# Kernel optimization log

Hardware: AMD Instinct MI355X
Metric: run time of the kernel (lower is better)

Reference implementation:

```python
import jax, jax.numpy as jnp
from jax import lax
import numpy as np

LATENT = 512
LABEL = 128
BATCH = 1024


def _maxpool2(x):
    # 2x2 max pool, stride 2, NCHW
    return lax.reduce_window(x, -jnp.inf, lax.max, (1, 1, 2, 2), (1, 1, 2, 2), 'VALID')


def _encoder(x, c1w, c1b, c2w, c2b, fw, fb):
    dn = ('NCHW', 'OIHW', 'NCHW')
    y = lax.conv_general_dilated(x, c1w, (1, 1), 'SAME', dimension_numbers=dn)
    y = _maxpool2(jax.nn.relu(y + c1b[None, :, None, None]))  # [B,32,14,14]
    y = lax.conv_general_dilated(y, c2w, (1, 1), 'SAME', dimension_numbers=dn)
    y = _maxpool2(jax.nn.relu(y + c2b[None, :, None, None]))  # [B,64,7,7]
    y = y.reshape(y.shape[0], -1)                              # [B,3136]
    return y @ fw.T + fb                                       # [B,latent]


def _hopfield_w(rep):
    # rho = mean over ALL elements (matches torch.mean(x))
    rho = jnp.mean(rep)
    t = rep - rho                      # [label, latent]
    w = t.T @ t                        # sum of rank-1 outer products
    w = w * (1.0 - jnp.eye(w.shape[0], dtype=w.dtype))  # zero diagonal
    return w / LABEL


def _clustering(lat, w):
    # batched fixed-length Hopfield relaxation with min-energy tracking
    s0 = jnp.tanh(lat)                 # [B,L]
    B = s0.shape[0]

    def step(carry, _):
        s, min_e, min_s = carry
        prev = lax.stop_gradient(s)    # torch detaches prev_s each iter
        s_new = jnp.abs(prev) * jnp.sign(prev @ w.T)      # [B,L]
        e = -jnp.einsum('bi,ij,bj->b', s_new, w, s_new)    # [B]
        better = e < min_e
        min_e = jnp.where(better, e, min_e)
        min_s = jnp.where(better[:, None], s_new, min_s)
        return (s_new, min_e, min_s), None

    init = (s0, jnp.full((B,), jnp.inf, dtype=s0.dtype), jnp.zeros_like(s0))
    (_, _, min_s), _ = lax.scan(step, init, None, length=LATENT)
    return min_s


def setup_inputs() -> dict:
    key = jax.random.key(0)
    ks = jax.random.split(key, 11)
    d = {}
    d['image'] = jax.random.normal(ks[0], (BATCH, 1, 28, 28), dtype=jnp.float32)
    d['label_images'] = jax.random.uniform(ks[1], (LABEL, 1, 28, 28), dtype=jnp.float32)
    d['conv1_w'] = jax.random.normal(ks[2], (32, 1, 5, 5), dtype=jnp.float32) * 0.1
    d['conv1_b'] = jnp.zeros((32,), dtype=jnp.float32)
    d['conv2_w'] = jax.random.normal(ks[3], (64, 32, 5, 5), dtype=jnp.float32) * 0.05
    d['conv2_b'] = jnp.zeros((64,), dtype=jnp.float32)
    d['fc1_w'] = jax.random.normal(ks[4], (LATENT, 64 * 7 * 7), dtype=jnp.float32) * 0.02
    d['fc1_b'] = jnp.zeros((LATENT,), dtype=jnp.float32)
    d['fcn_w'] = jax.random.normal(ks[5], (LABEL, LATENT), dtype=jnp.float32) * 0.05
    d['fcn_b'] = jnp.zeros((LABEL,), dtype=jnp.float32)
    return d


def reference(image, label_images, conv1_w, conv1_b, conv2_w, conv2_b,
              fc1_w, fc1_b, fcn_w, fcn_b):
    rep = jnp.tanh(_encoder(label_images, conv1_w, conv1_b, conv2_w, conv2_b, fc1_w, fc1_b))  # [label,L]
    lat = _encoder(image, conv1_w, conv1_b, conv2_w, conv2_b, fc1_w, fc1_b)                    # [B,L]
    # FCN on detached latents (torch: .clone().detach())
    label = jax.nn.softmax(lax.stop_gradient(lat) @ fcn_w.T + fcn_b, axis=1)                   # [B,label]
    w = _hopfield_w(rep)                                                                        # [L,L]
    min_s = _clustering(lat, w)                                                                 # [B,L]
    out = jax.nn.softmax(jnp.abs(min_s @ rep.T), axis=1)                                        # [B,label]
    return (out, label)
```

## Files before the change

### kernel.cpp

```cpp
#include <hip/hip_runtime.h>
#include <hip/hip_bf16.h>
#include <math.h>

#define BATCH 1024
#define LABEL 128
#define LATENT 512
#define NTOT 1152

typedef short short8 __attribute__((ext_vector_type(8)));
typedef float f32x16 __attribute__((ext_vector_type(16)));

__device__ __forceinline__ unsigned short f2bf(float f) {
    __hip_bfloat16 h = __float2bfloat16(f);
    return *(unsigned short*)&h;
}
__device__ __forceinline__ float bf2f(unsigned short u) {
    __hip_bfloat16 h; *(unsigned short*)&h = u;
    return __bfloat162float(h);
}

#define BSTR ((size_t)512 * 3136)
#define ASTR ((size_t)NTOT * 3136)
#define A2STR ((size_t)BATCH * 512)
#define W2STR ((size_t)LABEL * 512)


__global__ __launch_bounds__(256) void conv1_pool(const float* __restrict__ image,
                                                  const float* __restrict__ limg,
                                                  const float* __restrict__ wt,
                                                  const float* __restrict__ bias,
                                                  unsigned short* __restrict__ o1b) {
    const int n = blockIdx.x;
    const float* in = (n < BATCH) ? (image + (size_t)n * 784)
                                  : (limg + (size_t)(n - BATCH) * 784);
    __shared__ float pin[32][32];
    __shared__ float wts[32 * 25];
    const int tid = threadIdx.x;
    unsigned short* ob = o1b + (size_t)n * 12800;
    for (int i = tid; i < 256; i += 256) {
        int pl_ = i >> 7, r = i & 127;
        ob[pl_ * 6400 + 6272 + r] = 0;
    }
    for (int idx = tid; idx < 32 * 32; idx += 256) ((float*)pin)[idx] = 0.f;
    __syncthreads();
    for (int idx = tid; idx < 784; idx += 256) {
        int y = idx / 28, x = idx % 28;
        pin[y + 2][x + 2] = in[idx];
    }
    for (int idx = tid; idx < 800; idx += 256) wts[idx] = wt[idx];
    __syncthreads();
    const int oc = tid & 31;
    float wk[25];
    #pragma unroll
    for (int k = 0; k < 25; ++k) wk[k] = wts[oc * 25 + k];
    const float b = bias[oc];
    const int slot_lo = (oc & 7);
    const int gq = oc >> 3;
    for (int it = 0; it < 2; ++it) {
        const int py = (tid >> 5) + it * 8;
        if (py >= 14) continue;
        #pragma unroll
        for (int xh = 0; xh < 2; ++xh) {
            const int acol = xh ? 12 : 0;
            const int off = xh ? 2 : 0;
            float a0[14], a1[14];
            #pragma unroll
            for (int c = 0; c < 14; ++c) { a0[c] = b; a1[c] = b; }
            #pragma unroll
            for (int t = 0; t < 6; ++t) {
                float row[20];
                const float4* rp = (const float4*)&pin[2 * py + t][acol];
                #pragma unroll
                for (int v = 0; v < 5; ++v) {
                    float4 f = rp[v];
                    row[4 * v] = f.x; row[4 * v + 1] = f.y;
                    row[4 * v + 2] = f.z; row[4 * v + 3] = f.w;
                }
                if (t < 5) {
                    #pragma unroll
                    for (int kx = 0; kx < 5; ++kx) {
                        float w0 = wk[t * 5 + kx];
                        #pragma unroll
                        for (int c = 0; c < 14; ++c)
                            a0[c] = fmaf(row[c + kx + off], w0, a0[c]);
                    }
                }
                if (t >= 1) {
                    #pragma unroll
                    for (int kx = 0; kx < 5; ++kx) {
                        float w1 = wk[(t - 1) * 5 + kx];
                        #pragma unroll
                        for (int c = 0; c < 14; ++c)
                            a1[c] = fmaf(row[c + kx + off], w1, a1[c]);
                    }
                }
            }
            #pragma unroll
            for (int px = 0; px < 7; ++px) {
                float v = fmaxf(fmaxf(a0[2 * px], a0[2 * px + 1]),
                                fmaxf(a1[2 * px], a1[2 * px + 1]));
                v = fmaxf(v, 0.f);
                unsigned short b1 = f2bf(v);
                unsigned short b2 = f2bf(v - bf2f(b1));
                int p = py * 14 + 7 * xh + px;
                int offo = p * 32 + (((gq ^ (p >> 1)) & 3) << 3) + slot_lo;
                ob[offo] = b1; ob[6400 + offo] = b2;
            }
        }
    }
}

__global__ __launch_bounds__(256) void prep(const float* __restrict__ c2w,
                                            const float* __restrict__ f1w,
                                            const float* __restrict__ fnw,
                                            unsigned short* __restrict__ Bf,
                                            unsigned short* __restrict__ Bw2,
                                            unsigned short* __restrict__ Bn2) {
    int idx = blockIdx.x * 256 + threadIdx.x;
    if (idx < 102400) {
        int j = idx & 7, lane = (idx >> 3) & 63, ocT = (idx >> 9) & 1, s = idx >> 10;
        int q = lane >> 5, nn = lane & 31;
        int k = 16 * s + 8 * q + j;
        int tap = k >> 5, ic = k & 31;
        int oc = 32 * ocT + nn;
        float v = c2w[oc * 800 + ic * 25 + tap];
        unsigned short b1 = f2bf(v);
        unsigned short b2 = f2bf(v - bf2f(b1));
        size_t base = ((size_t)(s * 2 + ocT) * 2) * 512 + lane * 8 + j;
        Bf[base] = b1; Bf[base + 512] = b2;
        return;
    }
    int i2 = idx - 102400;
    if (i2 < 512 * 3136) {
        float v = f1w[i2];
        unsigned short b1 = f2bf(v);
        unsigned short b2 = f2bf(v - bf2f(b1));
        Bw2[i2] = b1; Bw2[BSTR + i2] = b2;
        return;
    }
    int i3 = i2 - 512 * 3136;
    if (i3 >= 128 * 512) return;
    float v = fnw[i3];
    unsigned short b1 = f2bf(v);
    unsigned short b2 = f2bf(v - bf2f(b1));
    Bn2[i3] = b1; Bn2[W2STR + i3] = b2;
}

__global__ __launch_bounds__(256) void conv2_mfma(const unsigned short* __restrict__ o1b,
                                                  const unsigned short* __restrict__ Bf,
                                                  const float* __restrict__ bias,
                                                  unsigned short* __restrict__ out2) {
    const int n = blockIdx.x;
    __shared__ __align__(16) unsigned short pl[12800];
    const int tid = threadIdx.x;
    const int lane = tid & 63, wv = tid >> 6;
    const int ocT = wv & 1, mh = wv >> 1;

    {
        const float4* src = (const float4*)(o1b + (size_t)n * 12800);
        float4* dst = (float4*)pl;
        for (int i = tid; i < 1600; i += 256) dst[i] = src[i];
    }
    __syncthreads();

    const int m_ = lane & 31, q = lane >> 5;
    int ym[4], xm[4], mm[4], tvv[4];
    #pragma unroll
    for (int tt = 0; tt < 4; ++tt) {
        int t = 4 * mh + tt;
        tvv[tt] = (t < 7);
        int m = 32 * t + m_;
        mm[tt] = m;
        ym[tt] = m / 14;
        xm[tt] = m - 14 * ym[tt];
    }
    f32x16 acc[4];
    {
        float bs = bias[32 * ocT + m_];
        #pragma unroll
        for (int tt = 0; tt < 4; ++tt)
        #pragma unroll
        for (int r = 0; r < 16; ++r) acc[tt][r] = bs;
    }

    for (int s = 0; s < 50; ++s) {
        const unsigned short* bp = Bf + ((size_t)(s * 2 + ocT) * 2) * 512 + lane * 8;
        short8 b1 = *(const short8*)(bp);
        short8 b2 = *(const short8*)(bp + 512);
        int kb = 16 * s + 8 * q;
        int tap = kb >> 5, ic0 = kb & 31, g = ic0 >> 3;
        int ky = (tap * 13) >> 6;
        int kx = tap - ky * 5;
        int iyk = ky - 2, ixk = kx - 2;
        int pq2 = iyk * 14 + ixk;
        short8 a1[4], a2[4];
        #pragma unroll
        for (int tt = 0; tt < 4; ++tt) {
            int iy = ym[tt] + iyk, ix = xm[tt] + ixk;
            int valid = tvv[tt] & ((unsigned)iy < 14u) & ((unsigned)ix < 14u);
            int cpt = valid ? (mm[tt] + pq2) : 196;
            int addr = cpt * 32 + (((g ^ (cpt >> 1)) & 3) << 3);
            a1[tt] = *(const short8*)(pl + addr);
            a2[tt] = *(const short8*)(pl + 6400 + addr);
        }
        #pragma unroll
        for (int tt = 0; tt < 4; ++tt)
            acc[tt] = __builtin_amdgcn_mfma_f32_32x32x16_bf16(a1[tt], b1, acc[tt], 0, 0, 0);
        #pragma unroll
        for (int tt = 0; tt < 4; ++tt)
            acc[tt] = __builtin_amdgcn_mfma_f32_32x32x16_bf16(a1[tt], b2, acc[tt], 0, 0, 0);
        #pragma unroll
        for (int tt = 0; tt < 4; ++tt)
            acc[tt] = __builtin_amdgcn_mfma_f32_32x32x16_bf16(a2[tt], b1, acc[tt], 0, 0, 0);
    }
    __syncthreads();

    float* hx = (float*)pl;
    {
        const int oc = 32 * ocT + m_;
        #pragma unroll
        for (int tt = 0; tt < 4; ++tt)
        #pragma unroll
        for (int e = 0; e < 8; ++e) {
            const int reg = 2 * e;
            const int r = (reg & 3) + 8 * (reg >> 2) + 4 * q;
            const int m = 32 * (4 * mh + tt) + r;
            if (m < 196) {
                float xm2 = fmaxf(acc[tt][reg], acc[tt][reg + 1]);
                int y = (m * 2341) >> 15;
                int px = (m - 14 * y) >> 1;
                hx[(y * 7 + px) * 65 + oc] = xm2;
            }
        }
    }
    __syncthreads();

    for (int idx = tid; idx < 3136; idx += 256) {
        int oc2 = (idx * 2675) >> 17;
        int p = idx - 49 * oc2;
        int py = (p * 9363) >> 16;
        int px = p - 7 * py;
        float v = fmaxf(hx[(2 * py * 7 + px) * 65 + oc2],
                        hx[((2 * py + 1) * 7 + px) * 65 + oc2]);
        v = fmaxf(v, 0.f);
        unsigned short b1 = f2bf(v);
        unsigned short b2 = f2bf(v - bf2f(b1));
        size_t o = (size_t)n * 3136 + idx;
        out2[o] = b1; out2[ASTR + o] = b2;
    }
}

__global__ __launch_bounds__(256) void fc1_mfma(const unsigned short* __restrict__ A2,
                                                const unsigned short* __restrict__ B2,
                                                float* __restrict__ part) {
    __shared__ unsigned short As[2][2048];
    __shared__ unsigned short Bs[2][2048];
    const int tid = threadIdx.x;
    const int n0 = blockIdx.x * 64, m0 = blockIdx.y * 64;
    const int koff = blockIdx.z * 448;
    const int lr = tid >> 2, g = tid & 3;
    const int slot = (((g ^ (lr >> 1)) & 3) << 3);
    const int lane = tid & 63, wv = tid >> 6;
    const int nq = wv & 1, mq = wv >> 1;
    const int q = lane >> 5, l31 = lane & 31;
    const int rA = 32 * nq + l31, rB = 32 * mq + l31;
    f32x16 acc;
    #pragma unroll
    for (int r = 0; r < 16; ++r) acc[r] = 0.f;

    for (int bk = 0; bk < 448; bk += 32) {
        const size_t ka = (size_t)(koff + bk + (g << 3));
        short8 av[2], bv[2];
        #pragma unroll
        for (int p = 0; p < 2; ++p) {
            av[p] = *(const short8*)(A2 + p * ASTR + (size_t)(n0 + lr) * 3136 + ka);
            bv[p] = *(const short8*)(B2 + p * BSTR + (size_t)(m0 + lr) * 3136 + ka);
        }
        __syncthreads();
        #pragma unroll
        for (int p = 0; p < 2; ++p) {
            *(short8*)&As[p][(lr << 5) + slot] = av[p];
            *(short8*)&Bs[p][(lr << 5) + slot] = bv[p];
        }
        __syncthreads();
        #pragma unroll
        for (int s2 = 0; s2 < 32; s2 += 16) {
            const int gg = (s2 + (q << 3)) >> 3;
            const int sa = (((gg ^ (rA >> 1)) & 3) << 3);
            const int sb = (((gg ^ (rB >> 1)) & 3) << 3);
            short8 a1 = *(const short8*)&As[0][(rA << 5) + sa];
            short8 a2 = *(const short8*)&As[1][(rA << 5) + sa];
            short8 b1 = *(const short8*)&Bs[0][(rB << 5) + sb];
            short8 b2 = *(const short8*)&Bs[1][(rB << 5) + sb];
            acc = __builtin_amdgcn_mfma_f32_32x32x16_bf16(a1, b1, acc, 0, 0, 0);
            acc = __builtin_amdgcn_mfma_f32_32x32x16_bf16(a1, b2, acc, 0, 0, 0);
            acc = __builtin_amdgcn_mfma_f32_32x32x16_bf16(a2, b1, acc, 0, 0, 0);
        }
    }
    float* pb = part + (size_t)blockIdx.z * NTOT * 512;
    #pragma unroll
    for (int reg = 0; reg < 16; ++reg) {
        int nn = n0 + 32 * nq + (reg & 3) + 8 * (reg >> 2) + 4 * q;
        int mmo = m0 + 32 * mq + l31;
        pb[(size_t)nn * 512 + mmo] = acc[reg];
    }
}

__global__ __launch_bounds__(256) void fc1_reduce(const float* __restrict__ part,
                                                  const float* __restrict__ bias,
                                                  float* __restrict__ lat,
                                                  unsigned short* __restrict__ lat2,
                                                  float* __restrict__ rep) {
    int idx = blockIdx.x * 256 + threadIdx.x;
    int m = idx & 511;
    float v = bias[m];
    #pragma unroll
    for (int kz = 0; kz < 7; ++kz) v += part[(size_t)kz * NTOT * 512 + idx];
    if (idx < BATCH * 512) {
        lat[idx] = v;
        unsigned short b1 = f2bf(v);
        lat2[idx] = b1;
        lat2[A2STR + idx] = f2bf(v - bf2f(b1));
    } else {
        rep[idx - BATCH * 512] = tanhf(v);
    }
}

__global__ __launch_bounds__(256) void fcn_mfma(const unsigned short* __restrict__ A2,
                                                const unsigned short* __restrict__ B2,
                                                float* __restrict__ logits) {
    __shared__ unsigned short As[2][2048];
    __shared__ unsigned short Bs[2][2048];
    const int tid = threadIdx.x;
    const int n0 = blockIdx.x * 64, m0 = blockIdx.y * 64;
    const int lr = tid >> 2, g = tid & 3;
    const int slot = (((g ^ (lr >> 1)) & 3) << 3);
    const int lane = tid & 63, wv = tid >> 6;
    const int nq = wv & 1, mq = wv >> 1;
    const int q = lane >> 5, l31 = lane & 31;
    const int rA = 32 * nq + l31, rB = 32 * mq + l31;
    f32x16 acc;
    #pragma unroll
    for (int r = 0; r < 16; ++r) acc[r] = 0.f;

    for (int bk = 0; bk < 512; bk += 32) {
        const size_t ka = (size_t)(bk + (g << 3));
        short8 av[2], bv[2];
        #pragma unroll
        for (int p = 0; p < 2; ++p) {
            av[p] = *(const short8*)(A2 + p * A2STR + (size_t)(n0 + lr) * 512 + ka);
            bv[p] = *(const short8*)(B2 + p * W2STR + (size_t)(m0 + lr) * 512 + ka);
        }
        __syncthreads();
        #pragma unroll
        for (int p = 0; p < 2; ++p) {
            *(short8*)&As[p][(lr << 5) + slot] = av[p];
            *(short8*)&Bs[p][(lr << 5) + slot] = bv[p];
        }
        __syncthreads();
        #pragma unroll
        for (int s2 = 0; s2 < 32; s2 += 16) {
            const int gg = (s2 + (q << 3)) >> 3;
            const int sa = (((gg ^ (rA >> 1)) & 3) << 3);
            const int sb = (((gg ^ (rB >> 1)) & 3) << 3);
            short8 a1 = *(const short8*)&As[0][(rA << 5) + sa];
            short8 a2 = *(const short8*)&As[1][(rA << 5) + sa];
            short8 b1 = *(const short8*)&Bs[0][(rB << 5) + sb];
            short8 b2 = *(const short8*)&Bs[1][(rB << 5) + sb];
            acc = __builtin_amdgcn_mfma_f32_32x32x16_bf16(a1, b1, acc, 0, 0, 0);
            acc = __builtin_amdgcn_mfma_f32_32x32x16_bf16(a1, b2, acc, 0, 0, 0);
            acc = __builtin_amdgcn_mfma_f32_32x32x16_bf16(a2, b1, acc, 0, 0, 0);
        }
    }
    #pragma unroll
    for (int reg = 0; reg < 16; ++reg) {
        int nn = n0 + 32 * nq + (reg & 3) + 8 * (reg >> 2) + 4 * q;
        int mmo = m0 + 32 * mq + l31;
        logits[(size_t)nn * 128 + mmo] = acc[reg];
    }
}

__global__ __launch_bounds__(128) void fcn_softmax2(const float* __restrict__ logits,
                                                    const float* __restrict__ fb,
                                                    float* __restrict__ out) {
    const int b = blockIdx.x;
    const int j = threadIdx.x;
    __shared__ float red[128];
    float acc = logits[(size_t)b * 128 + j] + fb[j];
    red[j] = acc;
    __syncthreads();
    for (int off = 64; off >= 1; off >>= 1) {
        if (j < off) red[j] = fmaxf(red[j], red[j + off]);
        __syncthreads();
    }
    float mx = red[0];
    __syncthreads();
    float ex = expf(acc - mx);
    red[j] = ex;
    __syncthreads();
    for (int off = 64; off >= 1; off >>= 1) {
        if (j < off) red[j] += red[j + off];
        __syncthreads();
    }
    out[(size_t)b * 128 + j] = ex / red[0];
}

__global__ __launch_bounds__(256) void rho_kernel(const float* __restrict__ rep,
                                                  float* __restrict__ rho) {
    __shared__ float red[256];
    const int tid = threadIdx.x;
    float s = 0.f;
    for (int i = tid; i < LABEL * LATENT; i += 256) s += rep[i];
    red[tid] = s;
    __syncthreads();
    for (int off = 128; off >= 1; off >>= 1) {
        if (tid < off) red[tid] += red[tid + off];
        __syncthreads();
    }
    if (tid == 0) rho[0] = red[0] / (float)(LABEL * LATENT);
}

__global__ __launch_bounds__(256) void t_kernel(const float* __restrict__ rep,
                                                const float* __restrict__ rho,
                                                float* __restrict__ tT) {
    int idx = blockIdx.x * 256 + threadIdx.x;
    int i = idx / 128, k = idx % 128;
    tT[idx] = rep[k * 512 + i] - rho[0];
}

__global__ __launch_bounds__(256) void w_kernel(const float* __restrict__ tT,
                                                float* __restrict__ w) {
    int idx = blockIdx.x * 256 + threadIdx.x;
    int i = idx >> 9, j = idx & 511;
    const float4* a = (const float4*)(tT + i * 128);
    const float4* b = (const float4*)(tT + j * 128);
    float acc = 0.f;
    #pragma unroll 8
    for (int q = 0; q < 32; ++q) {
        float4 av = a[q], bv = b[q];
        acc += av.x * bv.x + av.y * bv.y + av.z * bv.z + av.w * bv.w;
    }
    w[idx] = (i == j) ? 0.f : acc * (1.f / 128.f);
}

__global__ __launch_bounds__(256) void hinit(const float* __restrict__ lat,
                                             const float* __restrict__ w,
                                             float* __restrict__ hmat) {
    __shared__ float As[16][68];
    __shared__ float Bs[16][68];
    const int tid = threadIdx.x;
    const int n0 = blockIdx.x * 64, m0 = blockIdx.y * 64;
    const int lr = tid >> 2;
    const int lk = (tid & 3) * 4;
    const int ty = tid >> 4, tx = tid & 15;
    float c[4][4] = {};
    for (int k0 = 0; k0 < 512; k0 += 16) {
        float4 a4 = *(const float4*)(lat + (size_t)(n0 + lr) * 512 + k0 + lk);
        float4 b4 = *(const float4*)(w + (size_t)(m0 + lr) * 512 + k0 + lk);
        a4.x = tanhf(a4.x); a4.y = tanhf(a4.y); a4.z = tanhf(a4.z); a4.w = tanhf(a4.w);
        __syncthreads();
        As[lk + 0][lr] = a4.x; As[lk + 1][lr] = a4.y; As[lk + 2][lr] = a4.z; As[lk + 3][lr] = a4.w;
        Bs[lk + 0][lr] = b4.x; Bs[lk + 1][lr] = b4.y; Bs[lk + 2][lr] = b4.z; Bs[lk + 3][lr] = b4.w;
        __syncthreads();
        #pragma unroll
        for (int kk = 0; kk < 16; ++kk) {
            float av[4], bv[4];
            #pragma unroll
            for (int i = 0; i < 4; ++i) av[i] = As[kk][ty * 4 + i];
            #pragma unroll
            for (int j = 0; j < 4; ++j) bv[j] = Bs[kk][tx * 4 + j];
            #pragma unroll
            for (int i = 0; i < 4; ++i)
            #pragma unroll
            for (int j = 0; j < 4; ++j) c[i][j] += av[i] * bv[j];
        }
    }
    #pragma unroll
    for (int i = 0; i < 4; ++i)
    #pragma unroll
    for (int j = 0; j < 4; ++j)
        hmat[(size_t)(n0 + ty * 4 + i) * 512 + m0 + tx * 4 + j] = c[i][j];
}

#define CB 2
__device__ __forceinline__ float sgnf(float x) {
    return (x > 0.f) ? 1.f : ((x < 0.f) ? -1.f : 0.f);
}

__global__ __launch_bounds__(256) void clustering(const float* __restrict__ lat,
                                                  const float* __restrict__ hmat,
                                                  const float* __restrict__ w,
                                                  const float* __restrict__ rep,
                                                  float* __restrict__ out) {
    const int tid = threadIdx.x;
    const int row0 = blockIdx.x * CB;
    __shared__ float mins[CB][512];
    __shared__ float red[256];
    __shared__ float part_e[4][CB];
    __shared__ int part_c[4];
    __shared__ float min_e[CB];
    __shared__ int copyf[CB];
    __shared__ int donef[CB];
    __shared__ int cnt[CB];
    __shared__ int jidx[CB][512];
    __shared__ float jdel[CB][512];
    const int i0 = 2 * tid, i1 = 2 * tid + 1;
    const int wave = tid >> 6, lane = tid & 63;

    float sm10[CB], sm11[CB], sm20[CB], sm21[CB], h0[CB], h1[CB];
    #pragma unroll
    for (int r = 0; r < CB; ++r) {
        float a = tanhf(lat[(row0 + r) * 512 + i0]);
        float b = tanhf(lat[(row0 + r) * 512 + i1]);
        sm10[r] = a; sm11[r] = b;
        sm20[r] = a; sm21[r] = b;
        h0[r] = hmat[(size_t)(row0 + r) * 512 + i0];
        h1[r] = hmat[(size_t)(row0 + r) * 512 + i1];
    }
    if (tid < CB) { min_e[tid] = INFINITY; donef[tid] = 0; cnt[tid] = 0; }
    __syncthreads();

    for (int k = 1; k <= 512; ++k) {
        float sn0[CB], sn1[CB];
        int cy = (1 << CB) - 1;
        #pragma unroll
        for (int r = 0; r < CB; ++r) {
            int dn = donef[r];
            if (dn) {
                sn0[r] = sm10[r]; sn1[r] = sm11[r];
            } else {
                sn0[r] = fabsf(sm10[r]) * sgnf(h0[r]);
                sn1[r] = fabsf(sm11[r]) * sgnf(h1[r]);
                if (!(sn0[r] == sm20[r] && sn1[r] == sm21[r])) cy &= ~(1 << r);
                if (sn0[r] != sm10[r]) {
                    int p = atomicAdd(&cnt[r], 1);
                    jidx[r][p] = i0; jdel[r][p] = sn0[r] - sm10[r];
                }
                if (sn1[r] != sm11[r]) {
                    int p = atomicAdd(&cnt[r], 1);
                    jidx[r][p] = i1; jdel[r][p] = sn1[r] - sm11[r];
                }
            }
        }
        #pragma unroll
        for (int m = 32; m >= 1; m >>= 1) cy &= __shfl_xor(cy, m, 64);
        if (lane == 0) part_c[wave] = cy;
        __syncthreads();

        #pragma unroll
        for (int r = 0; r < CB; ++r) {
            const int c = cnt[r];
            #pragma unroll 4
            for (int t = 0; t < c; ++t) {
                const int j = jidx[r][t];
                const float d = jdel[r][t];
                const float2 wvv = *(const float2*)(w + (size_t)j * 512 + i0);
                h0[r] = fmaf(d, wvv.x, h0[r]);
                h1[r] = fmaf(d, wvv.y, h1[r]);
            }
        }
        float ep[CB];
        #pragma unroll
        for (int r = 0; r < CB; ++r) ep[r] = sn0[r] * h0[r] + sn1[r] * h1[r];
        #pragma unroll
        for (int m = 32; m >= 1; m >>= 1) {
            #pragma unroll
            for (int r = 0; r < CB; ++r) ep[r] += __shfl_xor(ep[r], m, 64);
        }
        if (lane == 0) {
            #pragma unroll
            for (int r = 0; r < CB; ++r) part_e[wave][r] = ep[r];
        }
        __syncthreads();

        if (tid < CB) {
            int r = tid;
            if (!donef[r]) {
                float e = -(part_e[0][r] + part_e[1][r] + part_e[2][r] + part_e[3][r]);
                int better = e < min_e[r];
                if (better) min_e[r] = e;
                copyf[r] = better;
                int fl = part_c[0] & part_c[1] & part_c[2] & part_c[3];
                int fixedp = (cnt[r] == 0);
                int cyc = (k >= 2) && ((fl >> r) & 1);
                if (fixedp || cyc) donef[r] = 1;
            } else {
                copyf[r] = 0;
            }
            cnt[r] = 0;
        }
        __syncthreads();

        int alldone = 1;
        #pragma unroll
        for (int r = 0; r < CB; ++r) {
            if (copyf[r]) { mins[r][i0] = sn0[r]; mins[r][i1] = sn1[r]; }
            alldone &= donef[r];
            sm20[r] = sm10[r]; sm21[r] = sm11[r];
            sm10[r] = sn0[r];  sm11[r] = sn1[r];
        }
        if (alldone) break;
    }
    __syncthreads();

    const int j = tid & 127, half = tid >> 7;
    for (int r = 0; r < CB; ++r) {
        const float4* rr = (const float4*)(rep + (size_t)j * 512 + half * 256);
        const float4* ms = (const float4*)(&mins[r][half * 256]);
        float p = 0.f;
        #pragma unroll 8
        for (int q = 0; q < 64; ++q) {
            float4 rv = rr[q], mv = ms[q];
            p += rv.x * mv.x + rv.y * mv.y + rv.z * mv.z + rv.w * mv.w;
        }
        red[tid] = p;
        __syncthreads();
        float v = 0.f;
        if (tid < 128) { v = fabsf(red[tid] + red[tid + 128]); red[tid] = v; }
        __syncthreads();
        for (int off = 64; off >= 1; off >>= 1) {
            if (tid < off) red[tid] = fmaxf(red[tid], red[tid + off]);
            __syncthreads();
        }
        float mx = red[0];
        __syncthreads();
        float ex = 0.f;
        if (tid < 128) { ex = expf(v - mx); red[tid] = ex; }
        __syncthreads();
        for (int off = 64; off >= 1; off >>= 1) {
            if (tid < off) red[tid] += red[tid + off];
            __syncthreads();
        }
        if (tid < 128) out[(size_t)(row0 + r) * 128 + tid] = ex / red[0];
        __syncthreads();
    }
}

extern "C" void kernel_launch(void* const* d_in, const int* in_sizes, int n_in,
                              void* d_out, int out_size, void* d_ws, size_t ws_size,
                              hipStream_t stream) {
    const float* image = (const float*)d_in[0];
    const float* limg  = (const float*)d_in[1];
    const float* c1w   = (const float*)d_in[2];
    const float* c1b   = (const float*)d_in[3];
    const float* c2w   = (const float*)d_in[4];
    const float* c2b   = (const float*)d_in[5];
    const float* f1w   = (const float*)d_in[6];
    const float* f1b   = (const float*)d_in[7];
    const float* fnw   = (const float*)d_in[8];
    const float* fnb   = (const float*)d_in[9];
    float* out = (float*)d_out;
    float* ws  = (float*)d_ws;

    unsigned short* o1b  = (unsigned short*)ws;
    unsigned short* out2 = o1b + (size_t)NTOT * 12800;
    float* lat  = (float*)(out2 + 2 * ASTR);
    float* rep  = lat + (size_t)BATCH * 512;
    float* tT   = rep + (size_t)LABEL * 512;
    float* wmat = tT + (size_t)512 * 128;
    float* rho  = wmat + (size_t)512 * 512;
    unsigned short* Bw2   = (unsigned short*)(rho + 16);
    unsigned short* Bfrag = Bw2 + 2 * BSTR;
    float* hmat = (float*)(Bfrag + 102400);
    unsigned short* lat2 = (unsigned short*)(hmat + A2STR);
    unsigned short* fnw2 = lat2 + 2 * A2STR;
    float* logits = (float*)(fnw2 + 2 * W2STR);
    float* part = (float*)ws;

    const int prep_total = 102400 + 512 * 3136 + 128 * 512;
    hipLaunchKernelGGL(prep, dim3((prep_total + 255) / 256), dim3(256), 0, stream,
                       c2w, f1w, fnw, Bfrag, Bw2, fnw2);
    hipLaunchKernelGGL(conv1_pool, dim3(NTOT), dim3(256), 0, stream, image, limg, c1w, c1b, o1b);
    hipLaunchKernelGGL(conv2_mfma, dim3(NTOT), dim3(256), 0, stream, o1b, Bfrag, c2b, out2);
    hipLaunchKernelGGL(fc1_mfma, dim3(NTOT / 64, 512 / 64, 7), dim3(256), 0, stream,
                       out2, Bw2, part);
    hipLaunchKernelGGL(fc1_reduce, dim3(NTOT * 512 / 256), dim3(256), 0, stream,
                       part, f1b, lat, lat2, rep);
    hipLaunchKernelGGL(fcn_mfma, dim3(16, 2), dim3(256), 0, stream, lat2, fnw2, logits);
    hipLaunchKernelGGL(fcn_softmax2, dim3(BATCH), dim3(128), 0, stream, logits, fnb,
                       out + (size_t)BATCH * LABEL);
    hipLaunchKernelGGL(rho_kernel, dim3(1), dim3(256), 0, stream, rep, rho);
    hipLaunchKernelGGL(t_kernel, dim3(256), dim3(256), 0, stream, rep, rho, tT);
    hipLaunchKernelGGL(w_kernel, dim3(1024), dim3(256), 0, stream, tT, wmat);
    hipLaunchKernelGGL(hinit, dim3(BATCH / 64, 512 / 64), dim3(256), 0, stream, lat, wmat, hmat);
    hipLaunchKernelGGL(clustering, dim3(BATCH / CB), dim3(256), 0, stream,
                       lat, hmat, wmat, rep, out);
}
```

Before: 401.2 us.

## Process one batch row per clustering block and tile the transpose kernel

The clustering kernel now handles a single batch row per block instead of two, launching 1024 blocks. Each row can exit as soon as it converges rather than waiting for its partner row, and per-row bookkeeping in shared memory drops. The t_kernel transpose now goes through a padded shared-memory tile so both its reads and writes are coalesced. The cost is twice as many clustering blocks, with each block reloading the W rows it touches and doing its own setup and softmax tail.

Measured after the change: 398.8 us (median of 2 runs). Within noise of the previous version (-0.6%).

```diff
diff --git a/kernel.cpp b/kernel.cpp
--- a/kernel.cpp
+++ b/kernel.cpp
@@ -423,9 +423,22 @@
 __global__ __launch_bounds__(256) void t_kernel(const float* __restrict__ rep,
                                                 const float* __restrict__ rho,
                                                 float* __restrict__ tT) {
-    int idx = blockIdx.x * 256 + threadIdx.x;
-    int i = idx / 128, k = idx % 128;
-    tT[idx] = rep[k * 512 + i] - rho[0];
+    __shared__ float tile[64][65];
+    const int tid = threadIdx.x;
+    const int i0 = blockIdx.x * 64, k0 = blockIdx.y * 64;
+    const int tx = tid & 63, ty4 = tid >> 6;
+    const float r0 = rho[0];
+    #pragma unroll
+    for (int rr = 0; rr < 16; ++rr) {
+        int kk = ty4 * 16 + rr;
+        tile[kk][tx] = rep[(size_t)(k0 + kk) * 512 + i0 + tx];
+    }
+    __syncthreads();
+    #pragma unroll
+    for (int rr = 0; rr < 16; ++rr) {
+        int ii = ty4 * 16 + rr;
+        tT[(size_t)(i0 + ii) * 128 + k0 + tx] = tile[tx][ii] - r0;
+    }
 }
 
 __global__ __launch_bounds__(256) void w_kernel(const float* __restrict__ tT,
@@ -482,7 +495,6 @@
         hmat[(size_t)(n0 + ty * 4 + i) * 512 + m0 + tx * 4 + j] = c[i][j];
 }
 
-#define CB 2
 __device__ __forceinline__ float sgnf(float x) {
     return (x > 0.f) ? 1.f : ((x < 0.f) ? -1.f : 0.f);
 }
@@ -493,120 +505,89 @@
                                                   const float* __restrict__ rep,
                                                   float* __restrict__ out) {
     const int tid = threadIdx.x;
-    const int row0 = blockIdx.x * CB;
-    __shared__ float mins[CB][512];
+    const int row = blockIdx.x;
+    __shared__ float mins[512];
     __shared__ float red[256];
-    __shared__ float part_e[4][CB];
+    __shared__ float part_e[4];
     __shared__ int part_c[4];
-    __shared__ float min_e[CB];
-    __shared__ int copyf[CB];
-    __shared__ int donef[CB];
-    __shared__ int cnt[CB];
-    __shared__ int jidx[CB][512];
-    __shared__ float jdel[CB][512];
+    __shared__ float min_e_s;
+    __shared__ int copyf_s;
+    __shared__ int donef_s;
+    __shared__ int cnt_s;
+    __shared__ int jidx[512];
+    __shared__ float jdel[512];
     const int i0 = 2 * tid, i1 = 2 * tid + 1;
     const int wave = tid >> 6, lane = tid & 63;
 
-    float sm10[CB], sm11[CB], sm20[CB], sm21[CB], h0[CB], h1[CB];
-    #pragma unroll
-    for (int r = 0; r < CB; ++r) {
-        float a = tanhf(lat[(row0 + r) * 512 + i0]);
-        float b = tanhf(lat[(row0 + r) * 512 + i1]);
-        sm10[r] = a; sm11[r] = b;
-        sm20[r] = a; sm21[r] = b;
-        h0[r] = hmat[(size_t)(row0 + r) * 512 + i0];
-        h1[r] = hmat[(size_t)(row0 + r) * 512 + i1];
-    }
-    if (tid < CB) { min_e[tid] = INFINITY; donef[tid] = 0; cnt[tid] = 0; }
+    float sm10, sm11, sm20, sm21, h0, h1;
+    {
+        sm10 = tanhf(lat[(size_t)row * 512 + i0]);
+        sm11 = tanhf(lat[(size_t)row * 512 + i1]);
+        sm20 = sm10; sm21 = sm11;
+        h0 = hmat[(size_t)row * 512 + i0];
+        h1 = hmat[(size_t)row * 512 + i1];
+    }
+    if (tid == 0) { min_e_s = INFINITY; donef_s = 0; cnt_s = 0; }
     __syncthreads();
 
     for (int k = 1; k <= 512; ++k) {
-        float sn0[CB], sn1[CB];
-        int cy = (1 << CB) - 1;
-        #pragma unroll
-        for (int r = 0; r < CB; ++r) {
-            int dn = donef[r];
-            if (dn) {
-                sn0[r] = sm10[r]; sn1[r] = sm11[r];
-            } else {
-                sn0[r] = fabsf(sm10[r]) * sgnf(h0[r]);
-                sn1[r] = fabsf(sm11[r]) * sgnf(h1[r]);
-                if (!(sn0[r] == sm20[r] && sn1[r] == sm21[r])) cy &= ~(1 << r);
-                if (sn0[r] != sm10[r]) {
-                    int p = atomicAdd(&cnt[r], 1);
-                    jidx[r][p] = i0; jdel[r][p] = sn0[r] - sm10[r];
-                }
-                if (sn1[r] != sm11[r]) {
-                    int p = atomicAdd(&cnt[r], 1);
-                    jidx[r][p] = i1; jdel[r][p] = sn1[r] - sm11[r];
-                }
-            }
+        float sn0 = fabsf(sm10) * sgnf(h0);
+        float sn1 = fabsf(sm11) * sgnf(h1);
+        int cy = (sn0 == sm20 && sn1 == sm21) ? 1 : 0;
+        if (sn0 != sm10) {
+            int p = atomicAdd(&cnt_s, 1);
+            jidx[p] = i0; jdel[p] = sn0 - sm10;
+        }
+        if (sn1 != sm11) {
+            int p = atomicAdd(&cnt_s, 1);
+            jidx[p] = i1; jdel[p] = sn1 - sm11;
         }
         #pragma unroll
         for (int m = 32; m >= 1; m >>= 1) cy &= __shfl_xor(cy, m, 64);
         if (lane == 0) part_c[wave] = cy;
         __syncthreads();
 
-        #pragma unroll
-        for (int r = 0; r < CB; ++r) {
-            const int c = cnt[r];
-            #pragma unroll 4
+        {
+            const int c = cnt_s;
+            #pragma unroll 8
             for (int t = 0; t < c; ++t) {
-                const int j = jidx[r][t];
-                const float d = jdel[r][t];
+                const int j = jidx[t];
+                const float d = jdel[t];
                 const float2 wvv = *(const float2*)(w + (size_t)j * 512 + i0);
-                h0[r] = fmaf(d, wvv.x, h0[r]);
-                h1[r] = fmaf(d, wvv.y, h1[r]);
+                h0 = fmaf(d, wvv.x, h0);
+                h1 = fmaf(d, wvv.y, h1);
             }
         }
-        float ep[CB];
-        #pragma unroll
-        for (int r = 0; r < CB; ++r) ep[r] = sn0[r] * h0[r] + sn1[r] * h1[r];
-        #pragma unroll
-        for (int m = 32; m >= 1; m >>= 1) {
-            #pragma unroll
-            for (int r = 0; r < CB; ++r) ep[r] += __shfl_xor(ep[r], m, 64);
-        }
-        if (lane == 0) {
-            #pragma unroll
-            for (int r = 0; r < CB; ++r) part_e[wave][r] = ep[r];
-        }
-        __syncthreads();
-
-        if (tid < CB) {
-            int r = tid;
-            if (!donef[r]) {
-                float e = -(part_e[0][r] + part_e[1][r] + part_e[2][r] + part_e[3][r]);
-                int better = e < min_e[r];
-                if (better) min_e[r] = e;
-                copyf[r] = better;
-                int fl = part_c[0] & part_c[1] & part_c[2] & part_c[3];
-                int fixedp = (cnt[r] == 0);
-                int cyc = (k >= 2) && ((fl >> r) & 1);
-                if (fixedp || cyc) donef[r] = 1;
-            } else {
-                copyf[r] = 0;
-            }
-            cnt[r] = 0;
-        }
-        __syncthreads();
-
-        int alldone = 1;
-        #pragma unroll
-        for (int r = 0; r < CB; ++r) {
-            if (copyf[r]) { mins[r][i0] = sn0[r]; mins[r][i1] = sn1[r]; }
-            alldone &= donef[r];
-            sm20[r] = sm10[r]; sm21[r] = sm11[r];
-            sm10[r] = sn0[r];  sm11[r] = sn1[r];
-        }
-        if (alldone) break;
+        float ep = sn0 * h0 + sn1 * h1;
+        #pragma unroll
+        for (int m = 32; m >= 1; m >>= 1) ep += __shfl_xor(ep, m, 64);
+        if (lane == 0) part_e[wave] = ep;
+        __syncthreads();
+
+        if (tid == 0) {
+            float e = -(part_e[0] + part_e[1] + part_e[2] + part_e[3]);
+            int better = e < min_e_s;
+            if (better) min_e_s = e;
+            copyf_s = better;
+            int fl = part_c[0] & part_c[1] & part_c[2] & part_c[3];
+            int fixedp = (cnt_s == 0);
+            int cyc = (k >= 2) && fl;
+            if (fixedp || cyc) donef_s = 1;
+            cnt_s = 0;
+        }
+        __syncthreads();
+
+        if (copyf_s) { mins[i0] = sn0; mins[i1] = sn1; }
+        sm20 = sm10; sm21 = sm11;
+        sm10 = sn0;  sm11 = sn1;
+        if (donef_s) break;
     }
     __syncthreads();
 
     const int j = tid & 127, half = tid >> 7;
-    for (int r = 0; r < CB; ++r) {
+    {
         const float4* rr = (const float4*)(rep + (size_t)j * 512 + half * 256);
-        const float4* ms = (const float4*)(&mins[r][half * 256]);
+        const float4* ms = (const float4*)(&mins[half * 256]);
         float p = 0.f;
         #pragma unroll 8
         for (int q = 0; q < 64; ++q) {
@@ -631,8 +612,7 @@
             if (tid < off) red[tid] += red[tid + off];
             __syncthreads();
         }
-        if (tid < 128) out[(size_t)(row0 + r) * 128 + tid] = ex / red[0];
-        __syncthreads();
+        if (tid < 128) out[(size_t)row * 128 + tid] = ex / red[0];
     }
 }
 
@@ -680,9 +660,9 @@
     hipLaunchKernelGGL(fcn_softmax2, dim3(BATCH), dim3(128), 0, stream, logits, fnb,
                        out + (size_t)BATCH * LABEL);
     hipLaunchKernelGGL(rho_kernel, dim3(1), dim3(256), 0, stream, rep, rho);
-    hipLaunchKernelGGL(t_kernel, dim3(256), dim3(256), 0, stream, rep, rho, tT);
+    hipLaunchKernelGGL(t_kernel, dim3(8, 2), dim3(256), 0, stream, rep, rho, tT);
     hipLaunchKernelGGL(w_kernel, dim3(1024), dim3(256), 0, stream, tT, wmat);
     hipLaunchKernelGGL(hinit, dim3(BATCH / 64, 512 / 64), dim3(256), 0, stream, lat, wmat, hmat);
-    hipLaunchKernelGGL(clustering, dim3(BATCH / CB), dim3(256), 0, stream,
+    hipLaunchKernelGGL(clustering, dim3(BATCH), dim3(256), 0, stream,
                        lat, hmat, wmat, rep, out);
 }
```
